# Kernel tuning notes

Hardware: AMD Instinct MI355X
Metric: run time of the kernel (lower is better)

## Reference

```python
import jax, jax.numpy as jnp
import numpy as np

RATIO = 0.5  # SAGPooling ratio


def setup_inputs() -> dict:
    key = jax.random.key(0)
    ks = jax.random.split(key, 6)
    B, n, d, out_dim, Eg = 128, 512, 256, 256, 4096  # graphs, nodes/graph, feat, proj out, edges/graph
    N = B * n
    x = jax.random.normal(ks[0], (N, d), dtype=jnp.float32)
    # edges connect nodes within the same graph (contiguous node blocks)
    src = jax.random.randint(ks[1], (B, Eg), 0, n)
    dst = jax.random.randint(ks[2], (B, Eg), 0, n)
    off = (jnp.arange(B) * n)[:, None]
    edge_index = jnp.stack([(src + off).reshape(-1), (dst + off).reshape(-1)]).astype(jnp.int32)
    batch = jnp.repeat(jnp.arange(B), n).astype(jnp.int32)
    s = 1.0 / np.sqrt(d).astype(np.float32)
    w_rel = jax.random.normal(ks[3], (d, 1), dtype=jnp.float32) * s   # GraphConv lin_rel (has bias)
    b_rel = jnp.zeros((1,), dtype=jnp.float32)
    w_root = jax.random.normal(ks[4], (d, 1), dtype=jnp.float32) * s  # GraphConv lin_root (no bias)
    w_proj = jax.random.normal(ks[5], (d, out_dim), dtype=jnp.float32) * s  # projection Linear
    b_proj = jnp.zeros((out_dim,), dtype=jnp.float32)
    return {"x": x, "edge_index": edge_index, "batch": batch, "num_graphs": B,
            "w_rel": w_rel, "b_rel": b_rel, "w_root": w_root,
            "w_proj": w_proj, "b_proj": b_proj}


def reference(x, edge_index, batch, num_graphs, w_rel, b_rel, w_root, w_proj, b_proj):
    N, d = x.shape
    n = N // num_graphs                    # equal-size graphs
    k = int(np.ceil(RATIO * n))            # PyG topk: ceil(ratio * num_nodes)
    src, dst = edge_index[0], edge_index[1]
    # GraphConv(node_dim, 1): score_i = lin_rel(sum_{j->i} x_j) + lin_root(x_i)
    agg = jax.ops.segment_sum(x[src], dst, num_segments=N)          # [N, d]
    score = jnp.tanh((agg @ w_rel + b_rel + x @ w_root)[:, 0])       # [N], tanh nonlinearity
    sb = score.reshape(num_graphs, n)                                # [B, n]
    top_vals, top_idx = jax.lax.top_k(sb, k)                         # per-graph topk
    xb = x.reshape(num_graphs, n, d)
    x_sel = jnp.take_along_axis(xb, top_idx[:, :, None], axis=1)     # [B, k, d]
    x_sel = x_sel * top_vals[:, :, None]                             # x[perm] * score[perm] (multiplier=1)
    pooled = x_sel.mean(axis=1)                                      # global_mean_pool over k kept nodes
    return pooled @ w_proj + b_proj                                  # [B, out_dim]
```

## Files before the change

kernel.cpp:

```cpp
#include <hip/hip_runtime.h>

#define D        256
#define NPG      512
#define BG       128
#define KSEL     256
#define EPG      4096
#define NN       (BG * NPG)
#define ET       (BG * EPG)

__global__ __launch_bounds__(256) void k_proj_scores(
        const float* __restrict__ x,
        const float* __restrict__ w_rel, const float* __restrict__ w_root,
        float* __restrict__ p, float* __restrict__ r) {
    int tid  = threadIdx.x;
    int wave = tid >> 6, lane = tid & 63;
    int node = blockIdx.x * 4 + wave;

    const float4* x4  = (const float4*)(x + (size_t)node * D);
    const float4* wr4 = (const float4*)w_rel;
    const float4* wo4 = (const float4*)w_root;
    float4 xv = x4[lane];
    float4 wr = wr4[lane];
    float4 wo = wo4[lane];
    float pv = xv.x * wr.x + xv.y * wr.y + xv.z * wr.z + xv.w * wr.w;
    float rv = xv.x * wo.x + xv.y * wo.y + xv.z * wo.z + xv.w * wo.w;
    #pragma unroll
    for (int off = 32; off; off >>= 1) {
        pv += __shfl_xor(pv, off, 64);
        rv += __shfl_xor(rv, off, 64);
    }
    if (lane == 0) { p[node] = pv; r[node] = rv; }
}

__global__ __launch_bounds__(1024) void k_fused(
        const float* __restrict__ x, const int* __restrict__ ei,
        const float* __restrict__ p, const float* __restrict__ r,
        const float* __restrict__ b_rel,
        const float* __restrict__ w_proj, const float* __restrict__ b_proj,
        float* __restrict__ out) {
    __shared__ float s_p[NPG];
    __shared__ float s_r[NPG];
    __shared__ float s_agg[NPG];
    __shared__ float s_val[NPG];
    __shared__ int   s_cnt2[1024];
    __shared__ int   s_selid[KSEL];
    __shared__ float s_selv[KSEL];
    __shared__ float s_pool[D];
    __shared__ float s_red[4][D];
    __shared__ int   s_nsel;

    int b = blockIdx.x, tid = threadIdx.x;
    int base = b * NPG;

    if (tid < NPG) { s_p[tid] = p[base + tid]; s_agg[tid] = 0.f; }
    else           { int j = tid - NPG; s_r[j] = r[base + j]; }
    if (tid < D)   s_pool[tid] = 0.f;
    if (tid == 0)  s_nsel = 0;
    __syncthreads();

    const int* src = ei + (size_t)b * EPG;
    const int* dst = ei + ET + (size_t)b * EPG;
    #pragma unroll
    for (int e = tid; e < EPG; e += 1024)
        atomicAdd(&s_agg[dst[e] - base], s_p[src[e] - base]);
    __syncthreads();

    float brel = b_rel[0];
    if (tid < NPG)
        s_val[tid] = tanhf(s_agg[tid] + brel + s_r[tid]);
    __syncthreads();

    {
        int j = tid & (NPG - 1);
        int half = tid >> 9;
        float sv = s_val[j];
        int lo = half * 256;
        int c = 0;
        #pragma unroll 8
        for (int i = lo; i < lo + 256; ++i) {
            float o = s_val[i];
            c += (o > sv) || (o == sv && i < j);
        }
        s_cnt2[tid] = c;
    }
    __syncthreads();
    if (tid < NPG) {
        int rank = s_cnt2[tid] + s_cnt2[tid + NPG];
        if (rank < KSEL) {
            int pos = atomicAdd(&s_nsel, 1);
            s_selid[pos] = tid;
            s_selv[pos]  = s_val[tid];
        }
    }
    __syncthreads();

    {
        int wave = tid >> 6, lane = tid & 63;
        float4 acc = {0.f, 0.f, 0.f, 0.f};
        #pragma unroll 4
        for (int m = 0; m < 16; ++m) {
            int s   = wave * 16 + m;
            int row = s_selid[s];
            float v = s_selv[s];
            float4 xv = ((const float4*)(x + (size_t)(base + row) * D))[lane];
            acc.x += v * xv.x; acc.y += v * xv.y;
            acc.z += v * xv.z; acc.w += v * xv.w;
        }
        atomicAdd(&s_pool[lane * 4 + 0], acc.x);
        atomicAdd(&s_pool[lane * 4 + 1], acc.y);
        atomicAdd(&s_pool[lane * 4 + 2], acc.z);
        atomicAdd(&s_pool[lane * 4 + 3], acc.w);
    }
    __syncthreads();

    {
        int f = tid & (D - 1);
        int q = tid >> 8;
        float partial = 0.f;
        int k0 = q * 64;
        #pragma unroll 8
        for (int kk = k0; kk < k0 + 64; ++kk)
            partial += s_pool[kk] * w_proj[kk * D + f];
        s_red[q][f] = partial;
    }
    __syncthreads();
    if (tid < D)
        out[(size_t)b * D + tid] = b_proj[tid] +
            (s_red[0][tid] + s_red[1][tid] + s_red[2][tid] + s_red[3][tid]) * (1.0f / KSEL);
}

extern "C" void kernel_launch(void* const* d_in, const int* in_sizes, int n_in,
                              void* d_out, int out_size, void* d_ws, size_t ws_size,
                              hipStream_t stream) {
    const float* x      = (const float*)d_in[0];
    const int*   ei     = (const int*)d_in[1];
    const float* w_rel  = (const float*)d_in[4];
    const float* b_rel  = (const float*)d_in[5];
    const float* w_root = (const float*)d_in[6];
    const float* w_proj = (const float*)d_in[7];
    const float* b_proj = (const float*)d_in[8];
    float* out = (float*)d_out;

    float* p = (float*)d_ws;
    float* r = p + NN;

    k_proj_scores<<<NN / 4, 256, 0, stream>>>(x, w_rel, w_root, p, r);
    k_fused<<<BG, 1024, 0, stream>>>(x, ei, p, r, b_rel, w_proj, b_proj, out);
}
```

Before: 137.1 us.

## Fuse per-node score projection into per-graph pooling kernel

```diff
diff --git a/kernel.cpp b/kernel.cpp
--- a/kernel.cpp
+++ b/kernel.cpp
@@ -8,34 +8,10 @@
 #define NN       (BG * NPG)
 #define ET       (BG * EPG)
 
-__global__ __launch_bounds__(256) void k_proj_scores(
-        const float* __restrict__ x,
-        const float* __restrict__ w_rel, const float* __restrict__ w_root,
-        float* __restrict__ p, float* __restrict__ r) {
-    int tid  = threadIdx.x;
-    int wave = tid >> 6, lane = tid & 63;
-    int node = blockIdx.x * 4 + wave;
-
-    const float4* x4  = (const float4*)(x + (size_t)node * D);
-    const float4* wr4 = (const float4*)w_rel;
-    const float4* wo4 = (const float4*)w_root;
-    float4 xv = x4[lane];
-    float4 wr = wr4[lane];
-    float4 wo = wo4[lane];
-    float pv = xv.x * wr.x + xv.y * wr.y + xv.z * wr.z + xv.w * wr.w;
-    float rv = xv.x * wo.x + xv.y * wo.y + xv.z * wo.z + xv.w * wo.w;
-    #pragma unroll
-    for (int off = 32; off; off >>= 1) {
-        pv += __shfl_xor(pv, off, 64);
-        rv += __shfl_xor(rv, off, 64);
-    }
-    if (lane == 0) { p[node] = pv; r[node] = rv; }
-}
-
-__global__ __launch_bounds__(1024) void k_fused(
+__global__ __launch_bounds__(1024) void k_all(
         const float* __restrict__ x, const int* __restrict__ ei,
-        const float* __restrict__ p, const float* __restrict__ r,
-        const float* __restrict__ b_rel,
+        const float* __restrict__ w_rel, const float* __restrict__ b_rel,
+        const float* __restrict__ w_root,
         const float* __restrict__ w_proj, const float* __restrict__ b_proj,
         float* __restrict__ out) {
     __shared__ float s_p[NPG];
@@ -50,22 +26,49 @@
     __shared__ int   s_nsel;
 
     int b = blockIdx.x, tid = threadIdx.x;
+    int wave = tid >> 6, lane = tid & 63;
     int base = b * NPG;
 
-    if (tid < NPG) { s_p[tid] = p[base + tid]; s_agg[tid] = 0.f; }
-    else           { int j = tid - NPG; s_r[j] = r[base + j]; }
+    const int* srcp = ei + (size_t)b * EPG;
+    const int* dstp = ei + ET + (size_t)b * EPG;
+    int se[4], de[4];
+    #pragma unroll
+    for (int q = 0; q < 4; ++q) {
+        se[q] = srcp[tid + q * 1024];
+        de[q] = dstp[tid + q * 1024];
+    }
+    float brel = b_rel[0];
+
+    if (tid < NPG) s_agg[tid] = 0.f;
     if (tid < D)   s_pool[tid] = 0.f;
     if (tid == 0)  s_nsel = 0;
+
+    {
+        const float4* wr4 = (const float4*)w_rel;
+        const float4* wo4 = (const float4*)w_root;
+        float4 wr = wr4[lane];
+        float4 wo = wo4[lane];
+        #pragma unroll 4
+        for (int i = 0; i < 32; ++i) {
+            int node = wave * 32 + i;
+            float4 xv = ((const float4*)(x + (size_t)(base + node) * D))[lane];
+            float pv = xv.x * wr.x + xv.y * wr.y + xv.z * wr.z + xv.w * wr.w;
+            float rv = xv.x * wo.x + xv.y * wo.y + xv.z * wo.z + xv.w * wo.w;
+            #pragma unroll
+            for (int off = 32; off; off >>= 1) {
+                pv += __shfl_xor(pv, off, 64);
+                rv += __shfl_xor(rv, off, 64);
+            }
+            if (lane == 0) { s_p[node] = pv; s_r[node] = rv; }
+        }
+    }
     __syncthreads();
 
-    const int* src = ei + (size_t)b * EPG;
-    const int* dst = ei + ET + (size_t)b * EPG;
     #pragma unroll
-    for (int e = tid; e < EPG; e += 1024)
-        atomicAdd(&s_agg[dst[e] - base], s_p[src[e] - base]);
+    for (int q = 0; q < 4; ++q)
+        atomicAdd(&s_agg[de[q] - base], s_p[se[q] - base]);
     __syncthreads();
 
-    float brel = b_rel[0];
     if (tid < NPG)
         s_val[tid] = tanhf(s_agg[tid] + brel + s_r[tid]);
     __syncthreads();
@@ -95,7 +98,6 @@
     __syncthreads();
 
     {
-        int wave = tid >> 6, lane = tid & 63;
         float4 acc = {0.f, 0.f, 0.f, 0.f};
         #pragma unroll 4
         for (int m = 0; m < 16; ++m) {
@@ -141,9 +143,5 @@
     const float* b_proj = (const float*)d_in[8];
     float* out = (float*)d_out;
 
-    float* p = (float*)d_ws;
-    float* r = p + NN;
-
-    k_proj_scores<<<NN / 4, 256, 0, stream>>>(x, w_rel, w_root, p, r);
-    k_fused<<<BG, 1024, 0, stream>>>(x, ei, p, r, b_rel, w_proj, b_proj, out);
+    k_all<<<BG, 1024, 0, stream>>>(x, ei, w_rel, b_rel, w_root, w_proj, b_proj, out);
 }
```

New measurement: 152.9 us. 11.6% more time.
